# Kernel optimization log

Measured on AMD Instinct MI355X. Metric: run time of the kernel, lower is better.

The kernel has to match this reference:

```python
import jax, jax.numpy as jnp
import numpy as np

SEQ_LEN, BATCH = 512, 64
VOCAB, EMB, HID = 10000, 512, 512


def _lstm_layer(x, Wih, Whh, bih, bhh):
    # x: [T, B, in_dim]; PyTorch gate order: i, f, g, o
    T, B, _ = x.shape
    H = Whh.shape[1]
    b = bih + bhh
    # precompute input projections for all timesteps: [T, B, 4H]
    xW = jnp.einsum('tbe,ge->tbg', x, Wih) + b

    def step(carry, xt):
        h, c = carry
        gates = xt + h @ Whh.T  # [B, 4H]
        i, f, g, o = jnp.split(gates, 4, axis=-1)
        i = jax.nn.sigmoid(i)
        f = jax.nn.sigmoid(f)
        g = jnp.tanh(g)
        o = jax.nn.sigmoid(o)
        c = f * c + i * g
        h = o * jnp.tanh(c)
        return (h, c), h

    init = (jnp.zeros((B, H), x.dtype), jnp.zeros((B, H), x.dtype))
    _, ys = jax.lax.scan(step, init, xW)
    return ys  # [T, B, H]


def setup_inputs() -> dict:
    key = jax.random.key(0)
    ks = jax.random.split(key, 12)
    src = jax.random.randint(ks[0], (SEQ_LEN, BATCH), 0, VOCAB)
    sen_len = jax.random.randint(ks[1], (BATCH,), 1, SEQ_LEN + 1)
    s_e = 1.0 / np.sqrt(EMB)
    s_h = 1.0 / np.sqrt(HID)
    emb_table = jax.random.normal(ks[2], (VOCAB, EMB), jnp.float32) * s_e
    Wih0 = jax.random.uniform(ks[3], (4 * HID, EMB), jnp.float32, -s_h, s_h)
    Whh0 = jax.random.uniform(ks[4], (4 * HID, HID), jnp.float32, -s_h, s_h)
    bih0 = jax.random.uniform(ks[5], (4 * HID,), jnp.float32, -s_h, s_h)
    bhh0 = jax.random.uniform(ks[6], (4 * HID,), jnp.float32, -s_h, s_h)
    Wih1 = jax.random.uniform(ks[7], (4 * HID, HID), jnp.float32, -s_h, s_h)
    Whh1 = jax.random.uniform(ks[8], (4 * HID, HID), jnp.float32, -s_h, s_h)
    bih1 = jax.random.uniform(ks[9], (4 * HID,), jnp.float32, -s_h, s_h)
    bhh1 = jax.random.uniform(ks[10], (4 * HID,), jnp.float32, -s_h, s_h)
    return {"src": src, "sen_len": sen_len, "emb_table": emb_table,
            "Wih0": Wih0, "Whh0": Whh0, "bih0": bih0, "bhh0": bhh0,
            "Wih1": Wih1, "Whh1": Whh1, "bih1": bih1, "bhh1": bhh1}


def reference(src, sen_len, emb_table, Wih0, Whh0, bih0, bhh0, Wih1, Whh1, bih1, bhh1):
    # Vectorized embedding gather: [T, B, EMB]
    embedded = emb_table[src]
    # Two-layer LSTM (eval mode; inter-layer dropout inactive)
    h1 = _lstm_layer(embedded, Wih0, Whh0, bih0, bhh0)
    outputs = _lstm_layer(h1, Wih1, Whh1, bih1, bhh1)  # [T, B, HID]
    # Per-sequence last valid hidden state, concatenated into flat vector [B*HID]
    B = src.shape[1]
    ot = outputs[sen_len - 1, jnp.arange(B), :]  # [B, HID]
    return ot.reshape(-1)
```

## Files before the change

kernel.cpp:

```cpp
#include <hip/hip_runtime.h>

#define T_LEN 512
#define BATCH 64
#define HID   512
#define EMB   512
#define NWG   256
#define TPB   512
#define RING_SLOT (HID * BATCH)

struct GBar {
  int leaf[16 * 32];
  int root; int pad1[31];
  int epoch; int pad2[31];
  int gep[16 * 32];
};

__global__ void init_ws_kernel(int* ws, int n) {
  int stride = gridDim.x * blockDim.x;
  for (int i = blockIdx.x * blockDim.x + threadIdx.x; i < n; i += stride) ws[i] = 0;
}

__device__ __forceinline__ float sigm(float x)      { return 1.f / (1.f + __expf(-x)); }
__device__ __forceinline__ float tanh_fast(float x) { return 1.f - 2.f / (__expf(2.f * x) + 1.f); }

__device__ __forceinline__ void cstore(float* p, float v) {
  __hip_atomic_store(p, v, __ATOMIC_RELAXED, __HIP_MEMORY_SCOPE_AGENT);
}

template <int I, int N>
struct Issue16 {
  static __device__ __forceinline__ void go(float4* dst, const float* p) {
    asm volatile("global_load_dwordx4 %0, %1, off offset:%2 sc0 sc1"
                 : "=v"(dst[I]) : "v"(p), "i"(I * 256));
    Issue16<I + 1, N>::go(dst, p);
  }
};
template <int N>
struct Issue16<N, N> {
  static __device__ __forceinline__ void go(float4*, const float*) {}
};

#define WAIT_VM(n) do {                                     \
    __builtin_amdgcn_sched_barrier(0);                      \
    asm volatile("s_waitcnt vmcnt(" #n ")" ::: "memory");   \
    __builtin_amdgcn_sched_barrier(0);                      \
  } while (0)

#define DOT_ACC(a, xv, wv) \
  a = fmaf((xv).w, (wv).w, fmaf((xv).z, (wv).z, fmaf((xv).y, (wv).y, fmaf((xv).x, (wv).x, (a)))))
#define AXPY4(acc, s, v) do { \
  (acc).x = fmaf((s), (v).x, (acc).x); \
  (acc).y = fmaf((s), (v).y, (acc).y); \
  (acc).z = fmaf((s), (v).z, (acc).z); \
  (acc).w = fmaf((s), (v).w, (acc).w); } while (0)

__global__ __launch_bounds__(TPB, 2) void lstm_pipe(
    const int* __restrict__ src, const int* __restrict__ sen_len,
    const float* __restrict__ emb,
    const float* __restrict__ Wih0, const float* __restrict__ Whh0,
    const float* __restrict__ bih0, const float* __restrict__ bhh0,
    const float* __restrict__ Wih1, const float* __restrict__ Whh1,
    const float* __restrict__ bih1, const float* __restrict__ bhh1,
    float* __restrict__ out,
    int* __restrict__ barp, float* __restrict__ h0ring, float* __restrict__ h1ring)
{
  extern __shared__ char smem_raw[];
  float4* WlV  = (float4*)smem_raw;
  float*  part = (float*)(smem_raw + 65536);
  GBar* bar = (GBar*)barp;

  const int wg    = blockIdx.x;
  const int layer = wg >> 7;
  const int w     = wg & 127;
  const int tid   = threadIdx.x;
  const int kh    = tid >> 6;
  const int lane  = tid & 63;
  const int bg    = lane >> 2;
  const int rg    = lane & 3;
  const int b0    = bg << 2;
  const int k0    = kh << 7;

  const float* Wih = layer ? Wih1 : Wih0;
  const float* Whh = layer ? Whh1 : Whh0;

  for (int idx = tid; idx < 4096; idx += TPB) {
    int rowl = idx & 15;
    int kc   = idx >> 4;
    int q = rowl >> 2, rjj = rowl & 3;
    int grow = q * HID + (w << 2) + rjj;
    int k4 = kc << 2;
    float4 v;
    if (k4 < EMB) v = *(const float4*)(Wih + (size_t)grow * EMB + k4);
    else          v = *(const float4*)(Whh + (size_t)grow * HID + (k4 - EMB));
    WlV[kc * 16 + rowl] = v;
  }

  const int p_b  = tid & 63;
  const int p_jj = (tid >> 6) & 3;
  const int p_jg = (w << 2) + p_jj;
  float bias4[4] = {0.f, 0.f, 0.f, 0.f};
  float c = 0.f;
  int   slen = -2;
  if (tid < 256) {
#pragma unroll
    for (int q = 0; q < 4; ++q) {
      int r = q * HID + p_jg;
      bias4[q] = layer ? (bih1[r] + bhh1[r]) : (bih0[r] + bhh0[r]);
    }
    slen = sen_len[p_b];
  }
  __syncthreads();

  for (int s = 0; s <= T_LEN; ++s) {
    const bool active = (layer == 0) ? (s < T_LEN) : (s >= 1);
    if (active) {
      const int t = (layer == 0) ? s : (s - 1);
      float4 acc[4];
#pragma unroll
      for (int q = 0; q < 4; ++q) acc[q] = make_float4(0.f, 0.f, 0.f, 0.f);

      if (layer == 0 && kh < 4) {
        const int* st = src + t * BATCH + b0;
        const float* e0 = emb + (size_t)st[0] * EMB;
        const float* e1 = emb + (size_t)st[1] * EMB;
        const float* e2 = emb + (size_t)st[2] * EMB;
        const float* e3 = emb + (size_t)st[3] * EMB;
#pragma unroll 4
        for (int kk = 0; kk < 128; kk += 4) {
          const int k  = k0 + kk;
          const int kc = k >> 2;
          float4 x0 = *(const float4*)(e0 + k);
          float4 x1 = *(const float4*)(e1 + k);
          float4 x2 = *(const float4*)(e2 + k);
          float4 x3 = *(const float4*)(e3 + k);
#pragma unroll
          for (int q = 0; q < 4; ++q) {
            float4 wq = WlV[kc * 16 + (q << 2) + rg];
            DOT_ACC(acc[q].x, x0, wq);
            DOT_ACC(acc[q].y, x1, wq);
            DOT_ACC(acc[q].z, x2, wq);
            DOT_ACC(acc[q].w, x3, wq);
          }
        }
      } else {
        const float* xT;
        if (layer == 0) {
          xT = h0ring + ((s + 1) & 1) * RING_SLOT + (k0 - EMB) * BATCH;
        } else if (kh < 4) {
          xT = h0ring + ((s - 1) & 1) * RING_SLOT + k0 * BATCH;
        } else {
          xT = h1ring + ((s - 1) & 1) * RING_SLOT + (k0 - EMB) * BATCH;
        }
        const float* p = xT + b0;

        float4 xa[16], xb[16];
        Issue16<0, 16>::go(xa, p);
#pragma unroll
        for (int g = 0; g < 8; ++g) {
          float4* cur = (g & 1) ? xb : xa;
          float4* nxt = (g & 1) ? xa : xb;
          if (g < 7) {
            Issue16<0, 16>::go(nxt, p + (g + 1) * 16 * BATCH);
            WAIT_VM(16);
          } else {
            WAIT_VM(0);
          }
#pragma unroll
          for (int ib = 0; ib < 4; ++ib) {
            const int kc = (k0 + (g << 4) + (ib << 2)) >> 2;
#pragma unroll
            for (int q = 0; q < 4; ++q) {
              float4 wq = WlV[kc * 16 + (q << 2) + rg];
              AXPY4(acc[q], wq.x, cur[(ib << 2) + 0]);
              AXPY4(acc[q], wq.y, cur[(ib << 2) + 1]);
              AXPY4(acc[q], wq.z, cur[(ib << 2) + 2]);
              AXPY4(acc[q], wq.w, cur[(ib << 2) + 3]);
            }
          }
        }
      }
#pragma unroll
      for (int q = 0; q < 4; ++q)
        *(float4*)(part + (kh << 10) + (((q << 2) + rg) << 6) + b0) = acc[q];
    }

    __syncthreads();

    if (active && tid < 256) {
      float g4[4];
#pragma unroll
      for (int q = 0; q < 4; ++q) {
        float a = bias4[q];
        const int base = (((q << 2) + p_jj) << 6) + p_b;
#pragma unroll
        for (int kk = 0; kk < 8; ++kk) a += part[(kk << 10) + base];
        g4[q] = a;
      }
      float ig = sigm(g4[0]), fg = sigm(g4[1]), gg = tanh_fast(g4[2]), og = sigm(g4[3]);
      c = fmaf(fg, c, ig * gg);
      float h = og * tanh_fast(c);
      float* ring = (layer == 0 ? h0ring : h1ring) + (s & 1) * RING_SLOT;
      cstore(ring + p_jg * BATCH + p_b, h);
      if (layer == 1) {
        const int t = s - 1;
        if (t == slen - 1) out[p_b * HID + p_jg] = h;
      }
    }

    __syncthreads();
    if (tid == 0) {
      const int target = s + 1;
      int* leafp = &bar->leaf[(wg >> 4) * 32];
      int* gepp  = &bar->gep[(wg >> 4) * 32];
      int prev = __hip_atomic_fetch_add(leafp, 1, __ATOMIC_RELAXED, __HIP_MEMORY_SCOPE_AGENT);
      if ((prev & 15) == 15) {
        int r = __hip_atomic_fetch_add(&bar->root, 1, __ATOMIC_RELAXED, __HIP_MEMORY_SCOPE_AGENT);
        if ((r & 15) == 15) {
          __hip_atomic_store(&bar->epoch, target, __ATOMIC_RELAXED, __HIP_MEMORY_SCOPE_AGENT);
        } else {
          while (__hip_atomic_load(&bar->epoch, __ATOMIC_RELAXED, __HIP_MEMORY_SCOPE_AGENT) < target)
            __builtin_amdgcn_s_sleep(1);
        }
        __hip_atomic_store(gepp, target, __ATOMIC_RELAXED, __HIP_MEMORY_SCOPE_AGENT);
      } else {
        while (__hip_atomic_load(gepp, __ATOMIC_RELAXED, __HIP_MEMORY_SCOPE_AGENT) < target)
          __builtin_amdgcn_s_sleep(1);
      }
    }
    __syncthreads();
  }
}

extern "C" void kernel_launch(void* const* d_in, const int* in_sizes, int n_in,
                              void* d_out, int out_size, void* d_ws, size_t ws_size,
                              hipStream_t stream) {
  const int*   src  = (const int*)d_in[0];
  const int*   slen = (const int*)d_in[1];
  const float* emb  = (const float*)d_in[2];
  const float* Wih0 = (const float*)d_in[3];
  const float* Whh0 = (const float*)d_in[4];
  const float* bih0 = (const float*)d_in[5];
  const float* bhh0 = (const float*)d_in[6];
  const float* Wih1 = (const float*)d_in[7];
  const float* Whh1 = (const float*)d_in[8];
  const float* bih1 = (const float*)d_in[9];
  const float* bhh1 = (const float*)d_in[10];
  float* out = (float*)d_out;

  int*   bar    = (int*)d_ws;
  float* h0ring = (float*)((char*)d_ws + 8192);
  float* h1ring = h0ring + 2 * RING_SLOT;

  int zero_ints = (8192 + 4 * RING_SLOT * 4) / 4;
  hipLaunchKernelGGL(init_ws_kernel, dim3(64), dim3(256), 0, stream, (int*)d_ws, zero_ints);

  (void)hipFuncSetAttribute((const void*)lstm_pipe,
                            hipFuncAttributeMaxDynamicSharedMemorySize, 98304);

  hipLaunchKernelGGL(lstm_pipe, dim3(NWG), dim3(TPB), 98304, stream,
                     src, slen, emb, Wih0, Whh0, bih0, bhh0, Wih1, Whh1, bih1, bhh1,
                     out, bar, h0ring, h1ring);
}
```

Measured before the change: 6.016 ms.

## Repartition work so each workgroup owns 8 hidden units over half the batch

Each of the 128 workgroups per layer now handles 8 hidden units (32 gate rows) for 32 batch columns, instead of 4 hidden units for all 64 batch columns. The K split across waves drops from 8 to 4 chunks of 256, and ring loads become float2. Per-step h reads per workgroup are halved, and the cross-wave partial-sum reduction shrinks. The cost is twice the LDS for weights (144KB dynamic shared memory), which may limit residency and make LDS bank behaviour differ.

```diff
diff --git a/kernel.cpp b/kernel.cpp
--- a/kernel.cpp
+++ b/kernel.cpp
@@ -28,16 +28,16 @@
 }
 
 template <int I, int N>
-struct Issue16 {
-  static __device__ __forceinline__ void go(float4* dst, const float* p) {
-    asm volatile("global_load_dwordx4 %0, %1, off offset:%2 sc0 sc1"
+struct Issue16F2 {
+  static __device__ __forceinline__ void go(float2* dst, const float* p) {
+    asm volatile("global_load_dwordx2 %0, %1, off offset:%2 sc0 sc1"
                  : "=v"(dst[I]) : "v"(p), "i"(I * 256));
-    Issue16<I + 1, N>::go(dst, p);
+    Issue16F2<I + 1, N>::go(dst, p);
   }
 };
 template <int N>
-struct Issue16<N, N> {
-  static __device__ __forceinline__ void go(float4*, const float*) {}
+struct Issue16F2<N, N> {
+  static __device__ __forceinline__ void go(float2*, const float*) {}
 };
 
 #define WAIT_VM(n) do {                                     \
@@ -48,11 +48,9 @@
 
 #define DOT_ACC(a, xv, wv) \
   a = fmaf((xv).w, (wv).w, fmaf((xv).z, (wv).z, fmaf((xv).y, (wv).y, fmaf((xv).x, (wv).x, (a)))))
-#define AXPY4(acc, s, v) do { \
+#define AXPY2(acc, s, v) do { \
   (acc).x = fmaf((s), (v).x, (acc).x); \
-  (acc).y = fmaf((s), (v).y, (acc).y); \
-  (acc).z = fmaf((s), (v).z, (acc).z); \
-  (acc).w = fmaf((s), (v).w, (acc).w); } while (0)
+  (acc).y = fmaf((s), (v).y, (acc).y); } while (0)
 
 __global__ __launch_bounds__(TPB, 2) void lstm_pipe(
     const int* __restrict__ src, const int* __restrict__ sen_len,
@@ -66,48 +64,51 @@
 {
   extern __shared__ char smem_raw[];
   float4* WlV  = (float4*)smem_raw;
-  float*  part = (float*)(smem_raw + 65536);
+  float*  part = (float*)(smem_raw + 131072);
   GBar* bar = (GBar*)barp;
 
   const int wg    = blockIdx.x;
   const int layer = wg >> 7;
-  const int w     = wg & 127;
+  const int w7    = wg & 127;
+  const int jsl   = w7 >> 1;
+  const int bhalf = w7 & 1;
+  const int j0    = jsl << 3;
+  const int bbase = bhalf << 5;
   const int tid   = threadIdx.x;
-  const int kh    = tid >> 6;
-  const int lane  = tid & 63;
-  const int bg    = lane >> 2;
-  const int rg    = lane & 3;
-  const int b0    = bg << 2;
-  const int k0    = kh << 7;
+  const int kh    = tid >> 7;
+  const int lane7 = tid & 127;
+  const int bg    = lane7 >> 3;
+  const int rg    = lane7 & 7;
+  const int b0    = bbase + (bg << 1);
+  const int k0    = kh << 8;
 
   const float* Wih = layer ? Wih1 : Wih0;
   const float* Whh = layer ? Whh1 : Whh0;
 
-  for (int idx = tid; idx < 4096; idx += TPB) {
-    int rowl = idx & 15;
-    int kc   = idx >> 4;
-    int q = rowl >> 2, rjj = rowl & 3;
-    int grow = q * HID + (w << 2) + rjj;
+  for (int idx = tid; idx < 8192; idx += TPB) {
+    int r32 = idx & 31;
+    int kc  = idx >> 5;
+    int q = r32 >> 3, jj = r32 & 7;
+    int grow = q * HID + j0 + jj;
     int k4 = kc << 2;
     float4 v;
     if (k4 < EMB) v = *(const float4*)(Wih + (size_t)grow * EMB + k4);
     else          v = *(const float4*)(Whh + (size_t)grow * HID + (k4 - EMB));
-    WlV[kc * 16 + rowl] = v;
-  }
-
-  const int p_b  = tid & 63;
-  const int p_jj = (tid >> 6) & 3;
-  const int p_jg = (w << 2) + p_jj;
+    WlV[kc * 32 + r32] = v;
+  }
+
+  const int p_jj = tid >> 5;
+  const int p_bl = tid & 31;
   float bias4[4] = {0.f, 0.f, 0.f, 0.f};
   float c = 0.f;
   int   slen = -2;
   if (tid < 256) {
 #pragma unroll
     for (int q = 0; q < 4; ++q) {
-      int r = q * HID + p_jg;
+      int r = q * HID + j0 + p_jj;
       bias4[q] = layer ? (bih1[r] + bhh1[r]) : (bih0[r] + bhh0[r]);
     }
-    slen = sen_len[p_b];
+    slen = sen_len[bbase + p_bl];
   }
   __syncthreads();
 
@@ -115,52 +116,46 @@
     const bool active = (layer == 0) ? (s < T_LEN) : (s >= 1);
     if (active) {
       const int t = (layer == 0) ? s : (s - 1);
-      float4 acc[4];
-#pragma unroll
-      for (int q = 0; q < 4; ++q) acc[q] = make_float4(0.f, 0.f, 0.f, 0.f);
-
-      if (layer == 0 && kh < 4) {
+      float2 acc[4];
+#pragma unroll
+      for (int q = 0; q < 4; ++q) acc[q] = make_float2(0.f, 0.f);
+
+      if (layer == 0 && kh < 2) {
         const int* st = src + t * BATCH + b0;
         const float* e0 = emb + (size_t)st[0] * EMB;
         const float* e1 = emb + (size_t)st[1] * EMB;
-        const float* e2 = emb + (size_t)st[2] * EMB;
-        const float* e3 = emb + (size_t)st[3] * EMB;
 #pragma unroll 4
-        for (int kk = 0; kk < 128; kk += 4) {
+        for (int kk = 0; kk < 256; kk += 4) {
           const int k  = k0 + kk;
           const int kc = k >> 2;
           float4 x0 = *(const float4*)(e0 + k);
           float4 x1 = *(const float4*)(e1 + k);
-          float4 x2 = *(const float4*)(e2 + k);
-          float4 x3 = *(const float4*)(e3 + k);
 #pragma unroll
           for (int q = 0; q < 4; ++q) {
-            float4 wq = WlV[kc * 16 + (q << 2) + rg];
+            float4 wq = WlV[kc * 32 + (q << 3) + rg];
             DOT_ACC(acc[q].x, x0, wq);
             DOT_ACC(acc[q].y, x1, wq);
-            DOT_ACC(acc[q].z, x2, wq);
-            DOT_ACC(acc[q].w, x3, wq);
           }
         }
       } else {
         const float* xT;
         if (layer == 0) {
           xT = h0ring + ((s + 1) & 1) * RING_SLOT + (k0 - EMB) * BATCH;
-        } else if (kh < 4) {
+        } else if (kh < 2) {
           xT = h0ring + ((s - 1) & 1) * RING_SLOT + k0 * BATCH;
         } else {
           xT = h1ring + ((s - 1) & 1) * RING_SLOT + (k0 - EMB) * BATCH;
         }
         const float* p = xT + b0;
 
-        float4 xa[16], xb[16];
-        Issue16<0, 16>::go(xa, p);
-#pragma unroll
-        for (int g = 0; g < 8; ++g) {
-          float4* cur = (g & 1) ? xb : xa;
-          float4* nxt = (g & 1) ? xa : xb;
-          if (g < 7) {
-            Issue16<0, 16>::go(nxt, p + (g + 1) * 16 * BATCH);
+        float2 xa[16], xb[16];
+        Issue16F2<0, 16>::go(xa, p);
+#pragma unroll
+        for (int g = 0; g < 16; ++g) {
+          float2* cur = (g & 1) ? xb : xa;
+          float2* nxt = (g & 1) ? xa : xb;
+          if (g < 15) {
+            Issue16F2<0, 16>::go(nxt, p + (g + 1) * 16 * BATCH);
             WAIT_VM(16);
           } else {
             WAIT_VM(0);
@@ -170,18 +165,18 @@
             const int kc = (k0 + (g << 4) + (ib << 2)) >> 2;
 #pragma unroll
             for (int q = 0; q < 4; ++q) {
-              float4 wq = WlV[kc * 16 + (q << 2) + rg];
-              AXPY4(acc[q], wq.x, cur[(ib << 2) + 0]);
-              AXPY4(acc[q], wq.y, cur[(ib << 2) + 1]);
-              AXPY4(acc[q], wq.z, cur[(ib << 2) + 2]);
-              AXPY4(acc[q], wq.w, cur[(ib << 2) + 3]);
+              float4 wq = WlV[kc * 32 + (q << 3) + rg];
+              AXPY2(acc[q], wq.x, cur[(ib << 2) + 0]);
+              AXPY2(acc[q], wq.y, cur[(ib << 2) + 1]);
+              AXPY2(acc[q], wq.z, cur[(ib << 2) + 2]);
+              AXPY2(acc[q], wq.w, cur[(ib << 2) + 3]);
             }
           }
         }
       }
 #pragma unroll
       for (int q = 0; q < 4; ++q)
-        *(float4*)(part + (kh << 10) + (((q << 2) + rg) << 6) + b0) = acc[q];
+        *(float2*)(part + (kh << 10) + (((q << 3) + rg) << 5) + (bg << 1)) = acc[q];
     }
 
     __syncthreads();
@@ -191,19 +186,19 @@
 #pragma unroll
       for (int q = 0; q < 4; ++q) {
         float a = bias4[q];
-        const int base = (((q << 2) + p_jj) << 6) + p_b;
-#pragma unroll
-        for (int kk = 0; kk < 8; ++kk) a += part[(kk << 10) + base];
+        const int base = (((q << 3) + p_jj) << 5) + p_bl;
+#pragma unroll
+        for (int kk = 0; kk < 4; ++kk) a += part[(kk << 10) + base];
         g4[q] = a;
       }
       float ig = sigm(g4[0]), fg = sigm(g4[1]), gg = tanh_fast(g4[2]), og = sigm(g4[3]);
       c = fmaf(fg, c, ig * gg);
       float h = og * tanh_fast(c);
       float* ring = (layer == 0 ? h0ring : h1ring) + (s & 1) * RING_SLOT;
-      cstore(ring + p_jg * BATCH + p_b, h);
+      cstore(ring + (j0 + p_jj) * BATCH + bbase + p_bl, h);
       if (layer == 1) {
         const int t = s - 1;
-        if (t == slen - 1) out[p_b * HID + p_jg] = h;
+        if (t == slen - 1) out[(bbase + p_bl) * HID + j0 + p_jj] = h;
       }
     }
 
@@ -255,9 +250,9 @@
   hipLaunchKernelGGL(init_ws_kernel, dim3(64), dim3(256), 0, stream, (int*)d_ws, zero_ints);
 
   (void)hipFuncSetAttribute((const void*)lstm_pipe,
-                            hipFuncAttributeMaxDynamicSharedMemorySize, 98304);
-
-  hipLaunchKernelGGL(lstm_pipe, dim3(NWG), dim3(TPB), 98304, stream,
+                            hipFuncAttributeMaxDynamicSharedMemorySize, 147456);
+
+  hipLaunchKernelGGL(lstm_pipe, dim3(NWG), dim3(TPB), 147456, stream,
                      src, slen, emb, Wih0, Whh0, bih0, bhh0, Wih1, Whh1, bih1, bhh1,
                      out, bar, h0ring, h1ring);
 }
```

After: 8.721 ms. 45.0% more time.
